# Kernel tuning notes

Hardware: AMD Instinct MI355X
Metric: run time of the kernel (lower is better)

The kernel has to match this reference:

```python
import jax, jax.numpy as jnp
import numpy as np

DIM = 1024
NUM_EXPERTS = 8
TOP_K = 2
LOAD_BALANCE_WEIGHT = 0.01


def setup_inputs() -> dict:
    key = jax.random.key(0)
    ks = jax.random.split(key, 8)
    d, e, h = DIM, NUM_EXPERTS, 4 * DIM
    scale = 0.02
    return {
        "x": jax.random.normal(ks[0], (4, 2048, d), dtype=jnp.float32),
        "w_router": jax.random.normal(ks[1], (d, e), dtype=jnp.float32) * scale,
        "b_router": jnp.zeros((e,), dtype=jnp.float32),
        "w1": jax.random.normal(ks[2], (e, d, h), dtype=jnp.float32) * scale,
        "b1": jnp.zeros((e, h), dtype=jnp.float32),
        "w2": jax.random.normal(ks[3], (e, h, d), dtype=jnp.float32) * scale,
        "b2": jnp.zeros((e, d), dtype=jnp.float32),
    }


def reference(x, w_router, b_router, w1, b1, w2, b2):
    # x: [b, s, d]
    router_logits = jnp.einsum("bsd,de->bse", x, w_router) + b_router  # [b,s,E]
    probs = jax.nn.softmax(router_logits, axis=-1)
    routing_weights, selected_experts = jax.lax.top_k(probs, TOP_K)  # [b,s,K]
    routing_weights = routing_weights / routing_weights.sum(axis=-1, keepdims=True)

    output = jnp.zeros_like(x)
    for e in range(NUM_EXPERTS):
        # Dense per-expert MLP; tokens not routed to expert e get gate 0,
        # matching the masked scatter-add in the original module.
        h = jax.nn.gelu(jnp.einsum("bsd,dh->bsh", x, w1[e]) + b1[e], approximate=False)
        y = jnp.einsum("bsh,hd->bsd", h, w2[e]) + b2[e]
        gate = jnp.where(selected_experts == e, routing_weights, 0.0).sum(axis=-1)  # [b,s]
        output = output + y * gate[..., None]

    # Load-balance aux loss: var (unbiased, ddof=1) / mean of tokens-per-expert.
    one_hot = jax.nn.one_hot(selected_experts, NUM_EXPERTS, dtype=jnp.float32)  # [b,s,K,E]
    tokens_per_expert = one_hot.sum(axis=(0, 1, 2))  # [E]
    load_balance_loss = (jnp.var(tokens_per_expert, ddof=1) / tokens_per_expert.mean()) * LOAD_BALANCE_WEIGHT
    return output, load_balance_loss
```

## Files before the change

### kernel.cpp

```cpp
#include <hip/hip_runtime.h>
#include <math.h>

#define TOKENS 8192
#define DIM    1024
#define NEXP   8
#define HID    4096
#define TILE_M 128
#define MAX_TILES 136
#define BKS    32

#define BK     32
#define LDA    40
#define LDB    40

typedef __bf16 bf16x8 __attribute__((ext_vector_type(8)));
typedef float  f32x4  __attribute__((ext_vector_type(4)));
typedef unsigned int u32x4 __attribute__((ext_vector_type(4)));

__device__ __forceinline__ unsigned short f2bf(float f) {
  union { float f; unsigned u; } v; v.f = f;
  unsigned u = v.u + 0x7fffu + ((v.u >> 16) & 1u);
  return (unsigned short)(u >> 16);
}
__device__ __forceinline__ float gelu_f(float v) {
  return 0.5f * v * (1.f + erff(v * 0.7071067811865476f));
}
__device__ __forceinline__ void gload16(const void* g, void* l) {
  __builtin_amdgcn_global_load_lds(
      (const __attribute__((address_space(1))) void*)g,
      (__attribute__((address_space(3))) void*)l, 16, 0, 0);
}
__device__ __forceinline__ int xcd_swz(int id, int nwg) {
  int q = nwg >> 3, r = nwg & 7;
  int xcd = id & 7, rank = id >> 3;
  return (xcd < r) ? xcd * (q + 1) + rank : r * (q + 1) + (xcd - r) * q + rank;
}

__global__ __launch_bounds__(256) void k_router(
    const float* __restrict__ x, const float* __restrict__ wr,
    const float* __restrict__ br, int* __restrict__ sel,
    float* __restrict__ gates, int* __restrict__ counts,
    unsigned short* __restrict__ xb)
{
  int t = blockIdx.x * 4 + (threadIdx.x >> 6);
  int lane = threadIdx.x & 63;
  const float* xr = x + (size_t)t * DIM;
  unsigned short* xo = xb + (size_t)t * DIM;
  float acc[NEXP];
#pragma unroll
  for (int e = 0; e < NEXP; ++e) acc[e] = 0.f;
#pragma unroll
  for (int it = 0; it < 4; ++it) {
    int d = it * 256 + lane * 4;
    float4 xv = *(const float4*)(xr + d);
    ushort4 pk;
    pk.x = f2bf(xv.x); pk.y = f2bf(xv.y); pk.z = f2bf(xv.z); pk.w = f2bf(xv.w);
    *(ushort4*)(xo + d) = pk;
    float xs[4] = {xv.x, xv.y, xv.z, xv.w};
#pragma unroll
    for (int j = 0; j < 4; ++j) {
      float4 wa = *(const float4*)(wr + (size_t)(d + j) * NEXP);
      float4 wb = *(const float4*)(wr + (size_t)(d + j) * NEXP + 4);
      acc[0] += xs[j] * wa.x; acc[1] += xs[j] * wa.y;
      acc[2] += xs[j] * wa.z; acc[3] += xs[j] * wa.w;
      acc[4] += xs[j] * wb.x; acc[5] += xs[j] * wb.y;
      acc[6] += xs[j] * wb.z; acc[7] += xs[j] * wb.w;
    }
  }
#pragma unroll
  for (int off = 32; off >= 1; off >>= 1) {
#pragma unroll
    for (int e = 0; e < NEXP; ++e) acc[e] += __shfl_xor(acc[e], off);
  }
  if (lane == 0) {
    float l[NEXP];
#pragma unroll
    for (int e = 0; e < NEXP; ++e) l[e] = acc[e] + br[e];
    int e1 = 0; float v1 = l[0];
#pragma unroll
    for (int e = 1; e < NEXP; ++e) if (l[e] > v1) { v1 = l[e]; e1 = e; }
    int e2 = -1; float v2 = -1e30f;
#pragma unroll
    for (int e = 0; e < NEXP; ++e) {
      if (e == e1) continue;
      if (l[e] > v2) { v2 = l[e]; e2 = e; }
    }
    float g1 = 1.f / (1.f + expf(v2 - v1));
    sel[t * 2] = e1; sel[t * 2 + 1] = e2;
    gates[t * 2] = g1; gates[t * 2 + 1] = 1.f - g1;
    atomicAdd(&counts[e1], 1);
    atomicAdd(&counts[e2], 1);
  }
}

__global__ void k_setup(const int* __restrict__ counts, int* __restrict__ cursors,
                        int* __restrict__ ntiles_p, int* __restrict__ tile_expert,
                        int* __restrict__ tile_row0, int* __restrict__ pair_token,
                        float* __restrict__ pair_gate, float* __restrict__ loss_out)
{
  if (threadIdx.x != 0) return;
  int poff = 0, nt = 0;
  float var = 0.f;
  for (int e = 0; e < NEXP; ++e) {
    int c = counts[e];
    cursors[e] = poff;
    int ntl = (c + TILE_M - 1) / TILE_M;
    for (int i = 0; i < ntl; ++i) { tile_expert[nt] = e; tile_row0[nt] = poff + i * TILE_M; ++nt; }
    for (int r = poff + c; r < poff + ntl * TILE_M; ++r) { pair_token[r] = -1; pair_gate[r] = 0.f; }
    float d = (float)c - 2048.f;
    var += d * d;
    poff += ntl * TILE_M;
  }
  *ntiles_p = nt;
  var *= (1.f / 7.f);
  *loss_out = var * (1.f / 2048.f) * 0.01f;
}

__global__ __launch_bounds__(256) void k_bucket(
    const int* __restrict__ sel, const float* __restrict__ gates,
    int* __restrict__ cursors, int* __restrict__ pair_token, float* __restrict__ pair_gate)
{
  int t = blockIdx.x * 256 + threadIdx.x;
#pragma unroll
  for (int k = 0; k < 2; ++k) {
    int e = sel[t * 2 + k];
    int pos = atomicAdd(&cursors[e], 1);
    pair_token[pos] = t;
    pair_gate[pos] = gates[t * 2 + k];
  }
}

__global__ __launch_bounds__(256) void k_castwT(
    const float* __restrict__ w, unsigned short* __restrict__ wT, int K, int N)
{
  __shared__ unsigned short t[64][72];
  int e = blockIdx.z, n0 = blockIdx.x * 64, k0 = blockIdx.y * 64;
  int tid = threadIdx.x;
  int kr = tid >> 2, nc = (tid & 3) * 16;
  const float* src = w + ((size_t)e * K + k0 + kr) * N + n0 + nc;
#pragma unroll
  for (int j = 0; j < 4; ++j) {
    f32x4 v = *(const f32x4*)(src + j * 4);
#pragma unroll
    for (int q = 0; q < 4; ++q) t[nc + j * 4 + q][kr] = f2bf(v[q]);
  }
  __syncthreads();
  int nr = tid >> 2, kc = (tid & 3) * 16;
  unsigned short* dst = wT + ((size_t)e * N + n0 + nr) * K + k0 + kc;
  *(u32x4*)dst = *(const u32x4*)&t[nr][kc];
  *(u32x4*)(dst + 8) = *(const u32x4*)&t[nr][kc + 8];
}

__global__ __launch_bounds__(256) void k_gemm1n(
    const unsigned short* __restrict__ xb, const unsigned short* __restrict__ w1T,
    const float* __restrict__ b1, const int* __restrict__ pair_token,
    const int* __restrict__ tile_expert, const int* __restrict__ tile_row0,
    const int* __restrict__ ntiles_p, unsigned short* __restrict__ h, int chunk_base)
{
  const int NBn = HID / 128;
  const int nwg = gridDim.x;
  int newid = xcd_swz(blockIdx.x, nwg);
  int ltile = newid / NBn, nb = newid - ltile * NBn;
  int tile = chunk_base + ltile;
  if (tile >= *ntiles_p) return;
  const int e = tile_expert[tile];
  const int row0 = tile_row0[tile];
  const int n0 = nb * 128;
  const int tid = threadIdx.x;
  const int w = tid >> 6, lane = tid & 63;

  __shared__ unsigned short As[2][128 * BKS];
  __shared__ unsigned short Bs[2][128 * BKS];
  __shared__ int tok[128];

  if (tid < 128) { int t = pair_token[row0 + tid]; tok[tid] = (t < 0) ? 0 : t; }
  __syncthreads();

  const int sr = lane >> 2;
  const int kq = (lane & 3) * 8;
  const int ar1 = w * 32 + sr, ar2 = ar1 + 16;
  const unsigned short* ag1 = xb + (size_t)tok[ar1] * DIM + kq;
  const unsigned short* ag2 = xb + (size_t)tok[ar2] * DIM + kq;
  const unsigned short* bg1 = w1T + ((size_t)e * HID + n0 + ar1) * DIM + kq;
  const unsigned short* bg2 = w1T + ((size_t)e * HID + n0 + ar2) * DIM + kq;

  const int wm = (w & 1) * 64, wn = (w >> 1) * 64;
  const int lr = lane & 15, lk = lane >> 4;

  f32x4 acc[4][4];
#pragma unroll
  for (int mi = 0; mi < 4; ++mi)
#pragma unroll
    for (int ni = 0; ni < 4; ++ni) acc[mi][ni] = {0.f, 0.f, 0.f, 0.f};

  {
    unsigned short* la1 = &As[0][(w * 32) * BKS];
    unsigned short* la2 = &As[0][(w * 32 + 16) * BKS];
    unsigned short* lb1 = &Bs[0][(w * 32) * BKS];
    unsigned short* lb2 = &Bs[0][(w * 32 + 16) * BKS];
    gload16(ag1, la1); gload16(ag2, la2);
    gload16(bg1, lb1); gload16(bg2, lb2);
  }
  asm volatile("s_waitcnt vmcnt(0)" ::: "memory");
  __builtin_amdgcn_s_barrier();

  const int NT = DIM / BKS;
  int cur = 0;
#pragma unroll 2
  for (int t = 0; t < NT; ++t) {
    int nxt = cur ^ 1;
    if (t + 1 < NT) {
      int k1 = (t + 1) * BKS;
      gload16(ag1 + k1, &As[nxt][(w * 32) * BKS]);
      gload16(ag2 + k1, &As[nxt][(w * 32 + 16) * BKS]);
      gload16(bg1 + k1, &Bs[nxt][(w * 32) * BKS]);
      gload16(bg2 + k1, &Bs[nxt][(w * 32 + 16) * BKS]);
    }
    bf16x8 af[4], bfr[4];
#pragma unroll
    for (int mi = 0; mi < 4; ++mi)
      af[mi] = *(const bf16x8*)&As[cur][(wm + mi * 16 + lr) * BKS + lk * 8];
#pragma unroll
    for (int ni = 0; ni < 4; ++ni)
      bfr[ni] = *(const bf16x8*)&Bs[cur][(wn + ni * 16 + lr) * BKS + lk * 8];
    asm volatile("s_waitcnt lgkmcnt(0)" ::: "memory");
    __builtin_amdgcn_sched_barrier(0);
    __builtin_amdgcn_s_setprio(1);
#pragma unroll
    for (int mi = 0; mi < 4; ++mi)
#pragma unroll
      for (int ni = 0; ni < 4; ++ni)
        acc[mi][ni] = __builtin_amdgcn_mfma_f32_16x16x32_bf16(af[mi], bfr[ni], acc[mi][ni], 0, 0, 0);
    __builtin_amdgcn_s_setprio(0);
    asm volatile("s_waitcnt vmcnt(0)" ::: "memory");
    __builtin_amdgcn_s_barrier();
    cur = nxt;
  }

  const size_t tl = (size_t)(tile - chunk_base);
  float bia[4];
#pragma unroll
  for (int ni = 0; ni < 4; ++ni) bia[ni] = b1[(size_t)e * HID + n0 + wn + ni * 16 + lr];
#pragma unroll
  for (int mi = 0; mi < 4; ++mi)
#pragma unroll
    for (int r = 0; r < 4; ++r) {
      int m = wm + mi * 16 + lk * 4 + r;
#pragma unroll
      for (int ni = 0; ni < 4; ++ni) {
        int n = wn + ni * 16 + lr;
        h[(tl * TILE_M + m) * HID + n0 + n] = f2bf(gelu_f(acc[mi][ni][r] + bia[ni]));
      }
    }
}

__global__ __launch_bounds__(256) void k_gemm2n(
    const unsigned short* __restrict__ h, const unsigned short* __restrict__ w2T,
    const float* __restrict__ b2, const int* __restrict__ pair_token,
    const float* __restrict__ pair_gate,
    const int* __restrict__ tile_expert, const int* __restrict__ tile_row0,
    const int* __restrict__ ntiles_p, float* __restrict__ out, int chunk_base)
{
  const int NBn = DIM / 128;
  const int nwg = gridDim.x;
  int newid = xcd_swz(blockIdx.x, nwg);
  int ltile = newid / NBn, nb = newid - ltile * NBn;
  int tile = chunk_base + ltile;
  if (tile >= *ntiles_p) return;
  const int e = tile_expert[tile];
  const int row0 = tile_row0[tile];
  const int n0 = nb * 128;
  const int tid = threadIdx.x;
  const int w = tid >> 6, lane = tid & 63;

  __shared__ unsigned short As[2][128 * BKS];
  __shared__ unsigned short Bs[2][128 * BKS];
  __shared__ int tok[128];
  __shared__ float gat[128];

  if (tid < 128) { tok[tid] = pair_token[row0 + tid]; gat[tid] = pair_gate[row0 + tid]; }
  __syncthreads();

  const int sr = lane >> 2;
  const int kq = (lane & 3) * 8;
  const int ar1 = w * 32 + sr, ar2 = ar1 + 16;
  const size_t tl = (size_t)(tile - chunk_base);
  const unsigned short* ag1 = h + (tl * TILE_M + ar1) * HID + kq;
  const unsigned short* ag2 = h + (tl * TILE_M + ar2) * HID + kq;
  const unsigned short* bg1 = w2T + ((size_t)e * DIM + n0 + ar1) * HID + kq;
  const unsigned short* bg2 = w2T + ((size_t)e * DIM + n0 + ar2) * HID + kq;

  const int wm = (w & 1) * 64, wn = (w >> 1) * 64;
  const int lr = lane & 15, lk = lane >> 4;

  f32x4 acc[4][4];
#pragma unroll
  for (int mi = 0; mi < 4; ++mi)
#pragma unroll
    for (int ni = 0; ni < 4; ++ni) acc[mi][ni] = {0.f, 0.f, 0.f, 0.f};

  {
    gload16(ag1, &As[0][(w * 32) * BKS]);
    gload16(ag2, &As[0][(w * 32 + 16) * BKS]);
    gload16(bg1, &Bs[0][(w * 32) * BKS]);
    gload16(bg2, &Bs[0][(w * 32 + 16) * BKS]);
  }
  asm volatile("s_waitcnt vmcnt(0)" ::: "memory");
  __builtin_amdgcn_s_barrier();

  const int NT = HID / BKS;
  int cur = 0;
#pragma unroll 2
  for (int t = 0; t < NT; ++t) {
    int nxt = cur ^ 1;
    if (t + 1 < NT) {
      int k1 = (t + 1) * BKS;
      gload16(ag1 + k1, &As[nxt][(w * 32) * BKS]);
      gload16(ag2 + k1, &As[nxt][(w * 32 + 16) * BKS]);
      gload16(bg1 + k1, &Bs[nxt][(w * 32) * BKS]);
      gload16(bg2 + k1, &Bs[nxt][(w * 32 + 16) * BKS]);
    }
    bf16x8 af[4], bfr[4];
#pragma unroll
    for (int mi = 0; mi < 4; ++mi)
      af[mi] = *(const bf16x8*)&As[cur][(wm + mi * 16 + lr) * BKS + lk * 8];
#pragma unroll
    for (int ni = 0; ni < 4; ++ni)
      bfr[ni] = *(const bf16x8*)&Bs[cur][(wn + ni * 16 + lr) * BKS + lk * 8];
    asm volatile("s_waitcnt lgkmcnt(0)" ::: "memory");
    __builtin_amdgcn_sched_barrier(0);
    __builtin_amdgcn_s_setprio(1);
#pragma unroll
    for (int mi = 0; mi < 4; ++mi)
#pragma unroll
      for (int ni = 0; ni < 4; ++ni)
        acc[mi][ni] = __builtin_amdgcn_mfma_f32_16x16x32_bf16(af[mi], bfr[ni], acc[mi][ni], 0, 0, 0);
    __builtin_amdgcn_s_setprio(0);
    asm volatile("s_waitcnt vmcnt(0)" ::: "memory");
    __builtin_amdgcn_s_barrier();
    cur = nxt;
  }

  float bia[4];
#pragma unroll
  for (int ni = 0; ni < 4; ++ni) bia[ni] = b2[(size_t)e * DIM + n0 + wn + ni * 16 + lr];
#pragma unroll
  for (int mi = 0; mi < 4; ++mi)
#pragma unroll
    for (int r = 0; r < 4; ++r) {
      int m = wm + mi * 16 + lk * 4 + r;
      int t = tok[m];
      if (t >= 0) {
        float g = gat[m];
#pragma unroll
        for (int ni = 0; ni < 4; ++ni) {
          int n = wn + ni * 16 + lr;
          atomicAdd(out + (size_t)t * DIM + n0 + n, (acc[mi][ni][r] + bia[ni]) * g);
        }
      }
    }
}

__global__ __launch_bounds__(256) void k_gemm1(
    const unsigned short* __restrict__ xb, const float* __restrict__ w1,
    const float* __restrict__ b1, const int* __restrict__ pair_token,
    const int* __restrict__ tile_expert, const int* __restrict__ tile_row0,
    const int* __restrict__ ntiles_p, unsigned short* __restrict__ h, int chunk_base)
{
  int tile = chunk_base + blockIdx.y;
  if (tile >= *ntiles_p) return;
  const int e = tile_expert[tile];
  const int row0 = tile_row0[tile];
  const int n0 = blockIdx.x * 128;
  const int tid = threadIdx.x;

  __shared__ unsigned short As[TILE_M * LDA];
  __shared__ unsigned short Bs[128 * LDB];
  __shared__ int tok[TILE_M];

  if (tid < TILE_M) tok[tid] = pair_token[row0 + tid];
  __syncthreads();

  const int ar = tid >> 1, akh = (tid & 1) * 16;
  const int bk = tid >> 3, bnh = (tid & 7) * 16;
  const int bswz = tid & 3;
  const int wv = tid >> 6, lane = tid & 63;
  const int wm = (wv & 1) * 64, wn = (wv >> 1) * 64;
  const int lr = lane & 15, lk = lane >> 4;
  const int atok = tok[ar];

  f32x4 acc[4][4];
#pragma unroll
  for (int mi = 0; mi < 4; ++mi)
#pragma unroll
    for (int ni = 0; ni < 4; ++ni) acc[mi][ni] = {0.f, 0.f, 0.f, 0.f};

  const unsigned short* asrc = (atok >= 0) ? (xb + (size_t)atok * DIM + akh) : (const unsigned short*)0;
  const float* bsrc0 = w1 + ((size_t)e * DIM + bk) * HID + n0 + bnh;
  const int wcol = 8 * ((bk >> 3) ^ bswz) + (bk & 7);

  for (int k0 = 0; k0 < DIM; k0 += BK) {
    u32x4 av0 = {0, 0, 0, 0}, av1 = {0, 0, 0, 0};
    if (asrc) {
      av0 = *(const u32x4*)(asrc + k0);
      av1 = *(const u32x4*)(asrc + k0 + 8);
    }
    float bv[16];
    const float* bs = bsrc0 + (size_t)k0 * HID;
#pragma unroll
    for (int j = 0; j < 4; ++j) {
      f32x4 f = *(const f32x4*)(bs + j * 4);
      bv[j * 4 + 0] = f[0]; bv[j * 4 + 1] = f[1];
      bv[j * 4 + 2] = f[2]; bv[j * 4 + 3] = f[3];
    }
    __syncthreads();
    *(u32x4*)&As[ar * LDA + akh] = av0;
    *(u32x4*)&As[ar * LDA + akh + 8] = av1;
#pragma unroll
    for (int j = 0; j < 16; ++j)
      Bs[(bnh + j) * LDB + wcol] = f2bf(bv[j]);
    __syncthreads();

    bf16x8 af[4], bfr[4];
#pragma unroll
    for (int mi = 0; mi < 4; ++mi)
      af[mi] = *(const bf16x8*)&As[(wm + mi * 16 + lr) * LDA + lk * 8];
#pragma unroll
    for (int ni = 0; ni < 4; ++ni) {
      int pch = lk ^ (((wn >> 4) + ni) & 3);
      bfr[ni] = *(const bf16x8*)&Bs[(wn + ni * 16 + lr) * LDB + pch * 8];
    }
#pragma unroll
    for (int mi = 0; mi < 4; ++mi)
#pragma unroll
      for (int ni = 0; ni < 4; ++ni)
        acc[mi][ni] = __builtin_amdgcn_mfma_f32_16x16x32_bf16(af[mi], bfr[ni], acc[mi][ni], 0, 0, 0);
  }

  const size_t tl = (size_t)(tile - chunk_base);
#pragma unroll
  for (int mi = 0; mi < 4; ++mi)
#pragma unroll
    for (int ni = 0; ni < 4; ++ni)
#pragma unroll
      for (int r = 0; r < 4; ++r) {
        int m = wm + mi * 16 + (lane >> 4) * 4 + r;
        int n = wn + ni * 16 + (lane & 15);
        float v = acc[mi][ni][r] + b1[(size_t)e * HID + n0 + n];
        h[(tl * TILE_M + m) * HID + n0 + n] = f2bf(gelu_f(v));
      }
}

__global__ __launch_bounds__(256) void k_gemm2(
    const unsigned short* __restrict__ h, const float* __restrict__ w2,
    const float* __restrict__ b2, const int* __restrict__ pair_token,
    const float* __restrict__ pair_gate,
    const int* __restrict__ tile_expert, const int* __restrict__ tile_row0,
    const int* __restrict__ ntiles_p, float* __restrict__ out, int chunk_base)
{
  int tile = chunk_base + blockIdx.y;
  if (tile >= *ntiles_p) return;
  const int e = tile_expert[tile];
  const int row0 = tile_row0[tile];
  const int n0 = blockIdx.x * 128;
  const int tid = threadIdx.x;

  __shared__ unsigned short As[TILE_M * LDA];
  __shared__ unsigned short Bs[128 * LDB];
  __shared__ int tok[TILE_M];
  __shared__ float gat[TILE_M];

  if (tid < TILE_M) { tok[tid] = pair_token[row0 + tid]; gat[tid] = pair_gate[row0 + tid]; }
  __syncthreads();

  const int ar = tid >> 1, akh = (tid & 1) * 16;
  const int bk = tid >> 3, bnh = (tid & 7) * 16;
  const int bswz = tid & 3;
  const int wv = tid >> 6, lane = tid & 63;
  const int wm = (wv & 1) * 64, wn = (wv >> 1) * 64;
  const int lr = lane & 15, lk = lane >> 4;

  f32x4 acc[4][4];
#pragma unroll
  for (int mi = 0; mi < 4; ++mi)
#pragma unroll
    for (int ni = 0; ni < 4; ++ni) acc[mi][ni] = {0.f, 0.f, 0.f, 0.f};

  const size_t tl = (size_t)(tile - chunk_base);
  const unsigned short* asrc = h + (tl * TILE_M + ar) * HID + akh;
  const float* bsrc0 = w2 + ((size_t)e * HID + bk) * DIM + n0 + bnh;
  const int wcol = 8 * ((bk >> 3) ^ bswz) + (bk & 7);

  for (int k0 = 0; k0 < HID; k0 += BK) {
    u32x4 av0 = *(const u32x4*)(asrc + k0);
    u32x4 av1 = *(const u32x4*)(asrc + k0 + 8);
    float bv[16];
    const float* bs = bsrc0 + (size_t)k0 * DIM;
#pragma unroll
    for (int j = 0; j < 4; ++j) {
      f32x4 f = *(const f32x4*)(bs + j * 4);
      bv[j * 4 + 0] = f[0]; bv[j * 4 + 1] = f[1];
      bv[j * 4 + 2] = f[2]; bv[j * 4 + 3] = f[3];
    }
    __syncthreads();
    *(u32x4*)&As[ar * LDA + akh] = av0;
    *(u32x4*)&As[ar * LDA + akh + 8] = av1;
#pragma unroll
    for (int j = 0; j < 16; ++j)
      Bs[(bnh + j) * LDB + wcol] = f2bf(bv[j]);
    __syncthreads();

    bf16x8 af[4], bfr[4];
#pragma unroll
    for (int mi = 0; mi < 4; ++mi)
      af[mi] = *(const bf16x8*)&As[(wm + mi * 16 + lr) * LDA + lk * 8];
#pragma unroll
    for (int ni = 0; ni < 4; ++ni) {
      int pch = lk ^ (((wn >> 4) + ni) & 3);
      bfr[ni] = *(const bf16x8*)&Bs[(wn + ni * 16 + lr) * LDB + pch * 8];
    }
#pragma unroll
    for (int mi = 0; mi < 4; ++mi)
#pragma unroll
      for (int ni = 0; ni < 4; ++ni)
        acc[mi][ni] = __builtin_amdgcn_mfma_f32_16x16x32_bf16(af[mi], bfr[ni], acc[mi][ni], 0, 0, 0);
  }

#pragma unroll
  for (int mi = 0; mi < 4; ++mi)
#pragma unroll
    for (int ni = 0; ni < 4; ++ni)
#pragma unroll
      for (int r = 0; r < 4; ++r) {
        int m = wm + mi * 16 + (lane >> 4) * 4 + r;
        int n = wn + ni * 16 + (lane & 15);
        int t = tok[m];
        if (t >= 0) {
          float v = acc[mi][ni][r] + b2[(size_t)e * DIM + n0 + n];
          atomicAdd(out + (size_t)t * DIM + n0 + n, v * gat[m]);
        }
      }
}

extern "C" void kernel_launch(void* const* d_in, const int* in_sizes, int n_in,
                              void* d_out, int out_size, void* d_ws, size_t ws_size,
                              hipStream_t stream) {
  const float* x  = (const float*)d_in[0];
  const float* wr = (const float*)d_in[1];
  const float* br = (const float*)d_in[2];
  const float* w1 = (const float*)d_in[3];
  const float* b1 = (const float*)d_in[4];
  const float* w2 = (const float*)d_in[5];
  const float* b2 = (const float*)d_in[6];
  float* out = (float*)d_out;

  char* ws = (char*)d_ws;
  int*   counts      = (int*)(ws + 0);
  int*   cursors     = (int*)(ws + 64);
  int*   ntiles      = (int*)(ws + 128);
  int*   tile_expert = (int*)(ws + 256);
  int*   tile_row0   = (int*)(ws + 1024);
  int*   sel         = (int*)(ws + 4096);
  float* gates       = (float*)(ws + 4096 + 65536);
  int*   pair_token  = (int*)(ws + 4096 + 131072);
  float* pair_gate   = (float*)(ws + 4096 + 131072 + 69632);

  const size_t OFF_XB  = 274432;
  const size_t XB_SZ   = (size_t)TOKENS * DIM * 2;
  const size_t OFF_W1T = OFF_XB + XB_SZ;
  const size_t WT_SZ   = (size_t)NEXP * DIM * HID * 2;
  const size_t OFF_W2T = OFF_W1T + WT_SZ;
  const size_t OFF_HN  = OFF_W2T + WT_SZ;
  const size_t tile_bytes = (size_t)TILE_M * HID * 2;

  unsigned short* xb  = (unsigned short*)(ws + OFF_XB);

  hipMemsetAsync(d_out, 0, (size_t)out_size * sizeof(float), stream);
  hipMemsetAsync(counts, 0, 64, stream);

  hipLaunchKernelGGL(k_router, dim3(TOKENS / 4), dim3(256), 0, stream,
                     x, wr, br, sel, gates, counts, xb);
  hipLaunchKernelGGL(k_setup, dim3(1), dim3(64), 0, stream,
                     counts, cursors, ntiles, tile_expert, tile_row0,
                     pair_token, pair_gate, out + (size_t)out_size - 1);
  hipLaunchKernelGGL(k_bucket, dim3(TOKENS / 256), dim3(256), 0, stream,
                     sel, gates, cursors, pair_token, pair_gate);

  bool newpath = ws_size >= OFF_HN + tile_bytes;

  if (newpath) {
    unsigned short* w1T = (unsigned short*)(ws + OFF_W1T);
    unsigned short* w2T = (unsigned short*)(ws + OFF_W2T);
    unsigned short* h   = (unsigned short*)(ws + OFF_HN);

    hipLaunchKernelGGL(k_castwT, dim3(HID / 64, DIM / 64, NEXP), dim3(256), 0, stream,
                       w1, w1T, DIM, HID);
    hipLaunchKernelGGL(k_castwT, dim3(DIM / 64, HID / 64, NEXP), dim3(256), 0, stream,
                       w2, w2T, HID, DIM);

    long long avail = (long long)ws_size - (long long)OFF_HN;
    int tpc = (int)(avail / (long long)tile_bytes);
    if (tpc < 1) tpc = 1;
    if (tpc > MAX_TILES) tpc = MAX_TILES;
    int nchunks = (MAX_TILES + tpc - 1) / tpc;

    for (int c = 0; c < nchunks; ++c) {
      hipLaunchKernelGGL(k_gemm1n, dim3(tpc * (HID / 128)), dim3(256), 0, stream,
                         xb, w1T, b1, pair_token, tile_expert, tile_row0, ntiles, h, c * tpc);
      hipLaunchKernelGGL(k_gemm2n, dim3(tpc * (DIM / 128)), dim3(256), 0, stream,
                         h, w2T, b2, pair_token, pair_gate, tile_expert, tile_row0, ntiles, out, c * tpc);
    }
  } else {
    unsigned short* h = (unsigned short*)(ws + OFF_W1T);
    long long avail = (long long)ws_size - (long long)OFF_W1T;
    int tpc = (avail > 0) ? (int)(avail / (long long)tile_bytes) : 0;
    if (tpc < 1) tpc = 1;
    if (tpc > MAX_TILES) tpc = MAX_TILES;
    int nchunks = (MAX_TILES + tpc - 1) / tpc;

    for (int c = 0; c < nchunks; ++c) {
      hipLaunchKernelGGL(k_gemm1, dim3(HID / 128, tpc), dim3(256), 0, stream,
                         xb, w1, b1, pair_token, tile_expert, tile_row0, ntiles, h, c * tpc);
      hipLaunchKernelGGL(k_gemm2, dim3(DIM / 128, tpc), dim3(256), 0, stream,
                         h, w2, b2, pair_token, pair_gate, tile_expert, tile_row0, ntiles, out, c * tpc);
    }
  }
}
```

Baseline: 843.9 us.

## Swap MFMA operands for row-contiguous epilogues, tanh GELU, parallel pad fill

Swaps the A/B operands of the MFMA calls in both expert GEMMs so each lane holds four consecutive output columns. The GEMM1 epilogue can then write packed 4-element bf16 stores, and both epilogues load bias as float4. GELU switches from the erf form to a tanh approximation built from exp and a fast reciprocal, which cuts epilogue math but changes numerics slightly. The setup kernel now fills padding slots with 256 threads instead of one serial thread.

```diff
diff --git a/kernel.cpp b/kernel.cpp
--- a/kernel.cpp
+++ b/kernel.cpp
@@ -25,6 +25,13 @@
 __device__ __forceinline__ float gelu_f(float v) {
   return 0.5f * v * (1.f + erff(v * 0.7071067811865476f));
 }
+__device__ __forceinline__ float gelu_fast(float v) {
+  float t = v * v;
+  float y = 0.7978845608f * v * fmaf(t, 0.044715f, 1.0f);
+  y = fminf(y, 15.f);
+  float z = __expf(2.f * y);
+  return v * z * __builtin_amdgcn_rcpf(1.f + z);
+}
 __device__ __forceinline__ void gload16(const void* g, void* l) {
   __builtin_amdgcn_global_load_lds(
       (const __attribute__((address_space(1))) void*)g,
@@ -93,27 +100,38 @@
   }
 }
 
-__global__ void k_setup(const int* __restrict__ counts, int* __restrict__ cursors,
-                        int* __restrict__ ntiles_p, int* __restrict__ tile_expert,
-                        int* __restrict__ tile_row0, int* __restrict__ pair_token,
-                        float* __restrict__ pair_gate, float* __restrict__ loss_out)
-{
-  if (threadIdx.x != 0) return;
-  int poff = 0, nt = 0;
-  float var = 0.f;
+__global__ __launch_bounds__(256) void k_setup(
+    const int* __restrict__ counts, int* __restrict__ cursors,
+    int* __restrict__ ntiles_p, int* __restrict__ tile_expert,
+    int* __restrict__ tile_row0, int* __restrict__ pair_token,
+    float* __restrict__ pair_gate, float* __restrict__ loss_out)
+{
+  __shared__ int s_pad0[NEXP], s_pad1[NEXP];
+  int tid = threadIdx.x;
+  if (tid == 0) {
+    int poff = 0, nt = 0;
+    float var = 0.f;
+    for (int e = 0; e < NEXP; ++e) {
+      int c = counts[e];
+      cursors[e] = poff;
+      int ntl = (c + TILE_M - 1) / TILE_M;
+      for (int i = 0; i < ntl; ++i) { tile_expert[nt] = e; tile_row0[nt] = poff + i * TILE_M; ++nt; }
+      s_pad0[e] = poff + c;
+      s_pad1[e] = poff + ntl * TILE_M;
+      float d = (float)c - 2048.f;
+      var += d * d;
+      poff += ntl * TILE_M;
+    }
+    *ntiles_p = nt;
+    *loss_out = (var * (1.f / 7.f)) * (1.f / 2048.f) * 0.01f;
+  }
+  __syncthreads();
+#pragma unroll
   for (int e = 0; e < NEXP; ++e) {
-    int c = counts[e];
-    cursors[e] = poff;
-    int ntl = (c + TILE_M - 1) / TILE_M;
-    for (int i = 0; i < ntl; ++i) { tile_expert[nt] = e; tile_row0[nt] = poff + i * TILE_M; ++nt; }
-    for (int r = poff + c; r < poff + ntl * TILE_M; ++r) { pair_token[r] = -1; pair_gate[r] = 0.f; }
-    float d = (float)c - 2048.f;
-    var += d * d;
-    poff += ntl * TILE_M;
-  }
-  *ntiles_p = nt;
-  var *= (1.f / 7.f);
-  *loss_out = var * (1.f / 2048.f) * 0.01f;
+    for (int r = s_pad0[e] + tid; r < s_pad1[e]; r += 256) {
+      pair_token[r] = -1; pair_gate[r] = 0.f;
+    }
+  }
 }
 
 __global__ __launch_bounds__(256) void k_bucket(
@@ -194,12 +212,10 @@
     for (int ni = 0; ni < 4; ++ni) acc[mi][ni] = {0.f, 0.f, 0.f, 0.f};
 
   {
-    unsigned short* la1 = &As[0][(w * 32) * BKS];
-    unsigned short* la2 = &As[0][(w * 32 + 16) * BKS];
-    unsigned short* lb1 = &Bs[0][(w * 32) * BKS];
-    unsigned short* lb2 = &Bs[0][(w * 32 + 16) * BKS];
-    gload16(ag1, la1); gload16(ag2, la2);
-    gload16(bg1, lb1); gload16(bg2, lb2);
+    gload16(ag1, &As[0][(w * 32) * BKS]);
+    gload16(ag2, &As[0][(w * 32 + 16) * BKS]);
+    gload16(bg1, &Bs[0][(w * 32) * BKS]);
+    gload16(bg2, &Bs[0][(w * 32 + 16) * BKS]);
   }
   asm volatile("s_waitcnt vmcnt(0)" ::: "memory");
   __builtin_amdgcn_s_barrier();
@@ -230,7 +246,7 @@
     for (int mi = 0; mi < 4; ++mi)
 #pragma unroll
       for (int ni = 0; ni < 4; ++ni)
-        acc[mi][ni] = __builtin_amdgcn_mfma_f32_16x16x32_bf16(af[mi], bfr[ni], acc[mi][ni], 0, 0, 0);
+        acc[mi][ni] = __builtin_amdgcn_mfma_f32_16x16x32_bf16(bfr[ni], af[mi], acc[mi][ni], 0, 0, 0);
     __builtin_amdgcn_s_setprio(0);
     asm volatile("s_waitcnt vmcnt(0)" ::: "memory");
     __builtin_amdgcn_s_barrier();
@@ -238,20 +254,25 @@
   }
 
   const size_t tl = (size_t)(tile - chunk_base);
-  float bia[4];
-#pragma unroll
-  for (int ni = 0; ni < 4; ++ni) bia[ni] = b1[(size_t)e * HID + n0 + wn + ni * 16 + lr];
-#pragma unroll
-  for (int mi = 0; mi < 4; ++mi)
-#pragma unroll
-    for (int r = 0; r < 4; ++r) {
-      int m = wm + mi * 16 + lk * 4 + r;
-#pragma unroll
-      for (int ni = 0; ni < 4; ++ni) {
-        int n = wn + ni * 16 + lr;
-        h[(tl * TILE_M + m) * HID + n0 + n] = f2bf(gelu_f(acc[mi][ni][r] + bia[ni]));
-      }
-    }
+  f32x4 bv[4];
+#pragma unroll
+  for (int ni = 0; ni < 4; ++ni)
+    bv[ni] = *(const f32x4*)(b1 + (size_t)e * HID + n0 + wn + ni * 16 + lk * 4);
+#pragma unroll
+  for (int mi = 0; mi < 4; ++mi) {
+    int m = wm + mi * 16 + lr;
+    unsigned short* hrow = h + (tl * TILE_M + m) * HID + n0;
+#pragma unroll
+    for (int ni = 0; ni < 4; ++ni) {
+      int nb4 = wn + ni * 16 + lk * 4;
+      ushort4 pk;
+      pk.x = f2bf(gelu_fast(acc[mi][ni][0] + bv[ni][0]));
+      pk.y = f2bf(gelu_fast(acc[mi][ni][1] + bv[ni][1]));
+      pk.z = f2bf(gelu_fast(acc[mi][ni][2] + bv[ni][2]));
+      pk.w = f2bf(gelu_fast(acc[mi][ni][3] + bv[ni][3]));
+      *(ushort4*)(hrow + nb4) = pk;
+    }
+  }
 }
 
 __global__ __launch_bounds__(256) void k_gemm2n(
@@ -334,31 +355,33 @@
     for (int mi = 0; mi < 4; ++mi)
 #pragma unroll
       for (int ni = 0; ni < 4; ++ni)
-        acc[mi][ni] = __builtin_amdgcn_mfma_f32_16x16x32_bf16(af[mi], bfr[ni], acc[mi][ni], 0, 0, 0);
+        acc[mi][ni] = __builtin_amdgcn_mfma_f32_16x16x32_bf16(bfr[ni], af[mi], acc[mi][ni], 0, 0, 0);
     __builtin_amdgcn_s_setprio(0);
     asm volatile("s_waitcnt vmcnt(0)" ::: "memory");
     __builtin_amdgcn_s_barrier();
     cur = nxt;
   }
 
-  float bia[4];
-#pragma unroll
-  for (int ni = 0; ni < 4; ++ni) bia[ni] = b2[(size_t)e * DIM + n0 + wn + ni * 16 + lr];
-#pragma unroll
-  for (int mi = 0; mi < 4; ++mi)
-#pragma unroll
-    for (int r = 0; r < 4; ++r) {
-      int m = wm + mi * 16 + lk * 4 + r;
-      int t = tok[m];
-      if (t >= 0) {
-        float g = gat[m];
-#pragma unroll
-        for (int ni = 0; ni < 4; ++ni) {
-          int n = wn + ni * 16 + lr;
-          atomicAdd(out + (size_t)t * DIM + n0 + n, (acc[mi][ni][r] + bia[ni]) * g);
-        }
+  f32x4 bv[4];
+#pragma unroll
+  for (int ni = 0; ni < 4; ++ni)
+    bv[ni] = *(const f32x4*)(b2 + (size_t)e * DIM + n0 + wn + ni * 16 + lk * 4);
+#pragma unroll
+  for (int mi = 0; mi < 4; ++mi) {
+    int m = wm + mi * 16 + lr;
+    int t = tok[m];
+    if (t >= 0) {
+      float g = gat[m];
+      float* orow = out + (size_t)t * DIM + n0;
+#pragma unroll
+      for (int ni = 0; ni < 4; ++ni) {
+        int nb4 = wn + ni * 16 + lk * 4;
+#pragma unroll
+        for (int r = 0; r < 4; ++r)
+          atomicAdd(orow + nb4 + r, (acc[mi][ni][r] + bv[ni][r]) * g);
       }
     }
+  }
 }
 
 __global__ __launch_bounds__(256) void k_gemm1(
@@ -580,7 +603,7 @@
 
   hipLaunchKernelGGL(k_router, dim3(TOKENS / 4), dim3(256), 0, stream,
                      x, wr, br, sel, gates, counts, xb);
-  hipLaunchKernelGGL(k_setup, dim3(1), dim3(64), 0, stream,
+  hipLaunchKernelGGL(k_setup, dim3(1), dim3(256), 0, stream,
                      counts, cursors, ntiles, tile_expert, tile_row0,
                      pair_token, pair_gate, out + (size_t)out_size - 1);
   hipLaunchKernelGGL(k_bucket, dim3(TOKENS / 256), dim3(256), 0, stream,
```

New measurement: 956.9 us. 1.13x slower.
